# Optimization experiments

Measured on AMD Instinct MI355X. Metric: run time of the kernel, lower is better.

Reference implementation:

```python
import jax, jax.numpy as jnp
import numpy as np

CONV_DIMS = (-3, -2)   # spatial dims (channel-last layout)
RADIUS = (3, 3)        # window = 1 + 2*r = 7 per dim -> 49 cells
STEP = (1, 1)


def _unfold(x, dim, window, step):
    """torch.Tensor.unfold: dim -> out_len, window appended as last axis."""
    dim = dim % x.ndim
    n = x.shape[dim]
    starts = jnp.arange((n - window) // step + 1) * step          # [L]
    idx = starts[:, None] + jnp.arange(window)[None, :]           # [L, w]
    y = jnp.take(x, idx, axis=dim)                                # dim -> [L, w]
    return jnp.moveaxis(y, dim + 1, -1)                           # window axis to last


def _local_attention(x):
    # Unfold each conv dim; move its window axis to the front (as in the torch code).
    for i, r, s in zip(CONV_DIMS, RADIUS, STEP):
        x = _unfold(x, i, 1 + 2 * r, s)
        x = jnp.moveaxis(x, -1, 0)
    n_win = len(CONV_DIMS)
    cells = int(np.prod(x.shape[:n_win]))
    x = x.reshape((cells,) + x.shape[n_win:])      # [cells, B, H', W', C]
    center = cells // 2                            # spatial center of the window
    q = jnp.moveaxis(x[center:center + 1], 0, -2)  # [B, H', W', 1, C]
    k = jnp.moveaxis(jnp.concatenate([x[:center], x[center + 1:]], axis=0), 0, -2)  # [B,H',W',cells-1,C]
    d = q.shape[-1]
    scores = jnp.einsum('...qc,...kc->...qk', q, k) / jnp.sqrt(jnp.asarray(d, q.dtype))
    w = jax.nn.softmax(scores, axis=-1)
    out = jnp.einsum('...qk,...kc->...qc', w, k)   # keys double as values
    return out.squeeze(-2)                          # [B, H', W', C]


def setup_inputs() -> dict:
    key = jax.random.key(0)
    X = jax.random.normal(key, (4, 64, 64, 256), dtype=jnp.float32)
    return {"X": X}


def reference(X):
    return _local_attention(X)
```

## Files before the change

### kernel.cpp

```cpp
#include <hip/hip_runtime.h>
#include <hip/hip_bf16.h>

#define B_   4
#define H_   64
#define W_   64
#define C_   256
#define HO_  58
#define WO_  58
#define JT   4
#define GRID (B_ * HO_ * JT)
#define PERX (GRID / 8)
#define CH   136

typedef __attribute__((ext_vector_type(8))) short bf16x8;
typedef __attribute__((ext_vector_type(4))) float f32x4;

__device__ __forceinline__ unsigned pk2(float a, float b) {
    float2 t; t.x = a; t.y = b;
    __hip_bfloat162 h = __float22bfloat162_rn(t);
    union { __hip_bfloat162 h2; unsigned u; } cv; cv.h2 = h;
    return cv.u;
}

template <int CTRL>
__device__ __forceinline__ float dpp_add(float p) {
    int t = __builtin_amdgcn_update_dpp(0, __builtin_bit_cast(int, p),
                                        CTRL, 0xF, 0xF, true);
    return p + __builtin_bit_cast(float, t);
}

union FU { unsigned u[4]; bf16x8 f; };

__global__ __launch_bounds__(256, 2) void convnd_attn_kernel(const float* __restrict__ X,
                                                             float* __restrict__ out) {
    __shared__ unsigned short Kb[154 * CH];
    __shared__ float S[16 * 168];
    __shared__ float invS[16];
    __shared__ unsigned short Wt[7 * 16 * 32];

    const int sp = (blockIdx.x & 7) * PERX + (blockIdx.x >> 3);
    const int jt = sp & 3;
    const int t1 = sp >> 2;
    const int i  = t1 % HO_;
    const int b  = t1 / HO_;
    const int j0 = (jt == 3) ? 42 : jt * 16;

    const int tid  = threadIdx.x;
    const int wave = tid >> 6;
    const int lane = tid & 63;
    const int q4   = lane >> 4;
    const int m16  = lane & 15;
    const float* base = X + (size_t)b * H_ * W_ * C_;

    for (int z = tid; z < 7 * 16 * 32 / 2; z += 256) ((unsigned*)Wt)[z] = 0u;

    f32x4 accS[2][2];
    #pragma unroll
    for (int sl = 0; sl < 2; ++sl)
        #pragma unroll
        for (int nt = 0; nt < 2; ++nt)
            accS[sl][nt] = (f32x4){0.f, 0.f, 0.f, 0.f};

    #pragma unroll
    for (int p = 0; p < 2; ++p) {
        if (p) __syncthreads();
        for (int s = 0; s < 20; ++s) {
            const int e4 = s * 256 + tid;
            if (e4 < 154 * 32) {
                const int row = e4 >> 5;
                const int cw  = (e4 & 31) << 2;
                const int di  = (row * 187) >> 12;
                const int kx  = row - 22 * di;
                const float4 v = *(const float4*)&base[((size_t)((i + di) * W_ + (j0 + kx))) * C_ + (p << 7) + cw];
                uint2 u; u.x = pk2(v.x, v.y); u.y = pk2(v.z, v.w);
                *(uint2*)&Kb[row * CH + cw] = u;
            }
        }
        __syncthreads();

        bf16x8 aq[4];
        #pragma unroll
        for (int kk = 0; kk < 4; ++kk)
            aq[kk] = *(const bf16x8*)&Kb[(69 + m16) * CH + kk * 32 + q4 * 8];

        #pragma unroll
        for (int sl = 0; sl < 2; ++sl) {
            const int di = wave + sl * 4;
            if (di > 6) continue;
            #pragma unroll
            for (int nt = 0; nt < 2; ++nt) {
                const int n0 = nt * 6;
                #pragma unroll
                for (int kk = 0; kk < 4; ++kk) {
                    const bf16x8 bk = *(const bf16x8*)&Kb[(di * 22 + n0 + m16) * CH + kk * 32 + q4 * 8];
                    accS[sl][nt] = __builtin_amdgcn_mfma_f32_16x16x32_bf16(aq[kk], bk, accS[sl][nt], 0, 0, 0);
                }
            }
        }
    }

    #pragma unroll
    for (int sl = 0; sl < 2; ++sl) {
        const int di = wave + sl * 4;
        if (di > 6) continue;
        #pragma unroll
        for (int nt = 0; nt < 2; ++nt) {
            const int n0 = nt * 6;
            #pragma unroll
            for (int reg = 0; reg < 4; ++reg)
                S[(q4 * 4 + reg) * 168 + di * 24 + n0 + m16] = accS[sl][nt][reg] * 0.0625f;
        }
    }
    __syncthreads();

    const int px = wave * 4 + q4;
    float ev[4];
    float esum = 0.f;
    #pragma unroll
    for (int r = 0; r < 4; ++r) {
        const int cidx = m16 + r * 16;
        float e = 0.f;
        if (cidx < 49 && cidx != 24) {
            const int di = (cidx * 37) >> 8;
            const int dj = cidx - 7 * di;
            e = __expf(S[px * 168 + di * 24 + (px + dj)]);
        }
        ev[r] = e; esum += e;
    }
    esum = dpp_add<0x111>(esum);
    esum = dpp_add<0x112>(esum);
    esum = dpp_add<0x114>(esum);
    esum = dpp_add<0x118>(esum);
    if (m16 == 15) invS[px] = 1.f / esum;
    __syncthreads();
    {
        const float inv = invS[px];
        #pragma unroll
        for (int r = 0; r < 4; ++r) {
            const int cidx = m16 + r * 16;
            if (cidx < 49 && cidx != 24) {
                const int di = (cidx * 37) >> 8;
                const int dj = cidx - 7 * di;
                const unsigned wb = pk2(ev[r] * inv, 0.f);
                Wt[di * 512 + px * 32 + (px + dj)] = (unsigned short)(wb & 0xFFFFu);
            }
        }
    }
    __syncthreads();

    bf16x8 aw[7];
    #pragma unroll
    for (int di = 0; di < 7; ++di)
        aw[di] = *(const bf16x8*)&Wt[di * 512 + m16 * 32 + q4 * 8];

    const size_t ob = ((size_t)(b * HO_ + i) * WO_ + j0) * C_;
    #pragma unroll
    for (int nt = 0; nt < 4; ++nt) {
        const int c = wave * 64 + nt * 16 + m16;
        f32x4 acc = (f32x4){0.f, 0.f, 0.f, 0.f};
        #pragma unroll
        for (int di = 0; di < 7; ++di) {
            FU bu;
            if (q4 == 3) {
                bu.u[0] = 0u; bu.u[1] = 0u; bu.u[2] = 0u; bu.u[3] = 0u;
            } else {
                const float* rb = base + ((size_t)((i + di) * W_ + j0)) * C_ + c;
                float f[8];
                #pragma unroll
                for (int jj = 0; jj < 8; ++jj) {
                    const int kx  = q4 * 8 + jj;
                    const int kxc = (kx < 22) ? kx : 21;
                    f[jj] = rb[(size_t)kxc * C_];
                }
                bu.u[0] = pk2(f[0], f[1]); bu.u[1] = pk2(f[2], f[3]);
                bu.u[2] = pk2(f[4], f[5]); bu.u[3] = pk2(f[6], f[7]);
            }
            acc = __builtin_amdgcn_mfma_f32_16x16x32_bf16(aw[di], bu.f, acc, 0, 0, 0);
        }
        #pragma unroll
        for (int reg = 0; reg < 4; ++reg)
            out[ob + (size_t)(q4 * 4 + reg) * C_ + c] = acc[reg];
    }
}

extern "C" void kernel_launch(void* const* d_in, const int* in_sizes, int n_in,
                              void* d_out, int out_size, void* d_ws, size_t ws_size,
                              hipStream_t stream) {
    const float* X = (const float*)d_in[0];
    float* outp    = (float*)d_out;
    hipLaunchKernelGGL(convnd_attn_kernel, dim3(GRID), dim3(256), 0, stream, X, outp);
}
```

Measured before the change: 95.77 us.

## Rewrite tile as 8-column block with swizzled LDS keys reused for values

```diff
diff --git a/kernel.cpp b/kernel.cpp
--- a/kernel.cpp
+++ b/kernel.cpp
@@ -7,10 +7,8 @@
 #define C_   256
 #define HO_  58
 #define WO_  58
-#define JT   4
-#define GRID (B_ * HO_ * JT)
+#define GRID (B_ * HO_ * 8)
 #define PERX (GRID / 8)
-#define CH   136
 
 typedef __attribute__((ext_vector_type(8))) short bf16x8;
 typedef __attribute__((ext_vector_type(4))) float f32x4;
@@ -21,29 +19,27 @@
     union { __hip_bfloat162 h2; unsigned u; } cv; cv.h2 = h;
     return cv.u;
 }
-
-template <int CTRL>
-__device__ __forceinline__ float dpp_add(float p) {
-    int t = __builtin_amdgcn_update_dpp(0, __builtin_bit_cast(int, p),
-                                        CTRL, 0xF, 0xF, true);
-    return p + __builtin_bit_cast(float, t);
+__device__ __forceinline__ float bf16f(unsigned bits) {
+    return __builtin_bit_cast(float, bits << 16);
 }
-
+__device__ __forceinline__ int SWZ(int row, int e) {
+    return (row << 8) + ((((e) >> 3) ^ (row & 7)) << 3) + ((e) & 7);
+}
 union FU { unsigned u[4]; bf16x8 f; };
 
-__global__ __launch_bounds__(256, 2) void convnd_attn_kernel(const float* __restrict__ X,
+__global__ __launch_bounds__(256, 3) void convnd_attn_kernel(const float* __restrict__ X,
                                                              float* __restrict__ out) {
-    __shared__ unsigned short Kb[154 * CH];
-    __shared__ float S[16 * 168];
-    __shared__ float invS[16];
-    __shared__ unsigned short Wt[7 * 16 * 32];
+    __shared__ __align__(16) unsigned short Kb[98 * 256];
+    __shared__ __align__(16) unsigned short S16[98 * 8];
+    __shared__ __align__(16) unsigned short Wt[8 * 96];
+    __shared__ float Wtail[2 * 16];
 
     const int sp = (blockIdx.x & 7) * PERX + (blockIdx.x >> 3);
-    const int jt = sp & 3;
-    const int t1 = sp >> 2;
+    const int jt = sp & 7;
+    const int t1 = sp >> 3;
     const int i  = t1 % HO_;
     const int b  = t1 / HO_;
-    const int j0 = (jt == 3) ? 42 : jt * 16;
+    const int j0 = (jt == 7) ? 50 : jt * 8;
 
     const int tid  = threadIdx.x;
     const int wave = tid >> 6;
@@ -52,134 +48,135 @@
     const int m16  = lane & 15;
     const float* base = X + (size_t)b * H_ * W_ * C_;
 
-    for (int z = tid; z < 7 * 16 * 32 / 2; z += 256) ((unsigned*)Wt)[z] = 0u;
-
-    f32x4 accS[2][2];
-    #pragma unroll
-    for (int sl = 0; sl < 2; ++sl)
-        #pragma unroll
-        for (int nt = 0; nt < 2; ++nt)
-            accS[sl][nt] = (f32x4){0.f, 0.f, 0.f, 0.f};
-
-    #pragma unroll
-    for (int p = 0; p < 2; ++p) {
-        if (p) __syncthreads();
-        for (int s = 0; s < 20; ++s) {
-            const int e4 = s * 256 + tid;
-            if (e4 < 154 * 32) {
-                const int row = e4 >> 5;
-                const int cw  = (e4 & 31) << 2;
-                const int di  = (row * 187) >> 12;
-                const int kx  = row - 22 * di;
-                const float4 v = *(const float4*)&base[((size_t)((i + di) * W_ + (j0 + kx))) * C_ + (p << 7) + cw];
-                uint2 u; u.x = pk2(v.x, v.y); u.y = pk2(v.z, v.w);
-                *(uint2*)&Kb[row * CH + cw] = u;
-            }
-        }
-        __syncthreads();
-
-        bf16x8 aq[4];
-        #pragma unroll
-        for (int kk = 0; kk < 4; ++kk)
-            aq[kk] = *(const bf16x8*)&Kb[(69 + m16) * CH + kk * 32 + q4 * 8];
-
-        #pragma unroll
-        for (int sl = 0; sl < 2; ++sl) {
-            const int di = wave + sl * 4;
-            if (di > 6) continue;
-            #pragma unroll
-            for (int nt = 0; nt < 2; ++nt) {
-                const int n0 = nt * 6;
-                #pragma unroll
-                for (int kk = 0; kk < 4; ++kk) {
-                    const bf16x8 bk = *(const bf16x8*)&Kb[(di * 22 + n0 + m16) * CH + kk * 32 + q4 * 8];
-                    accS[sl][nt] = __builtin_amdgcn_mfma_f32_16x16x32_bf16(aq[kk], bk, accS[sl][nt], 0, 0, 0);
-                }
-            }
-        }
-    }
-
-    #pragma unroll
-    for (int sl = 0; sl < 2; ++sl) {
-        const int di = wave + sl * 4;
-        if (di > 6) continue;
-        #pragma unroll
-        for (int nt = 0; nt < 2; ++nt) {
-            const int n0 = nt * 6;
-            #pragma unroll
-            for (int reg = 0; reg < 4; ++reg)
-                S[(q4 * 4 + reg) * 168 + di * 24 + n0 + m16] = accS[sl][nt][reg] * 0.0625f;
+    #pragma unroll 5
+    for (int s = 0; s < 25; ++s) {
+        const int idx = s * 256 + tid;
+        if (idx < 6272) {
+            const int row = idx >> 6;
+            const int ch  = (idx & 63) << 2;
+            const int di  = (row * 2341) >> 15;
+            const int kx  = row - 14 * di;
+            const float4 v = *(const float4*)&base[((size_t)((i + di) * W_ + (j0 + kx))) * C_ + ch];
+            uint2 u; u.x = pk2(v.x, v.y); u.y = pk2(v.z, v.w);
+            *(uint2*)&Kb[SWZ(row, ch)] = u;
         }
     }
     __syncthreads();
 
-    const int px = wave * 4 + q4;
-    float ev[4];
-    float esum = 0.f;
+    const int rq = 45 + m16;
+    bf16x8 qf[8];
     #pragma unroll
-    for (int r = 0; r < 4; ++r) {
-        const int cidx = m16 + r * 16;
-        float e = 0.f;
-        if (cidx < 49 && cidx != 24) {
-            const int di = (cidx * 37) >> 8;
-            const int dj = cidx - 7 * di;
-            e = __expf(S[px * 168 + di * 24 + (px + dj)]);
+    for (int kk = 0; kk < 8; ++kk)
+        qf[kk] = *(const bf16x8*)&Kb[SWZ(rq, (kk << 5) + (q4 << 3))];
+
+    f32x4 accS[2];
+    accS[0] = (f32x4){0.f, 0.f, 0.f, 0.f};
+    accS[1] = (f32x4){0.f, 0.f, 0.f, 0.f};
+    #pragma unroll
+    for (int sl = 0; sl < 2; ++sl) {
+        const int di = wave + 4 * sl;
+        if (di > 6) continue;
+        const int rk = di * 14 + (m16 < 14 ? m16 : 13);
+        #pragma unroll
+        for (int kk = 0; kk < 8; ++kk) {
+            const bf16x8 kf_ = *(const bf16x8*)&Kb[SWZ(rk, (kk << 5) + (q4 << 3))];
+            accS[sl] = __builtin_amdgcn_mfma_f32_16x16x32_bf16(kf_, qf[kk], accS[sl], 0, 0, 0);
         }
-        ev[r] = e; esum += e;
     }
-    esum = dpp_add<0x111>(esum);
-    esum = dpp_add<0x112>(esum);
-    esum = dpp_add<0x114>(esum);
-    esum = dpp_add<0x118>(esum);
-    if (m16 == 15) invS[px] = 1.f / esum;
-    __syncthreads();
-    {
-        const float inv = invS[px];
+    #pragma unroll
+    for (int sl = 0; sl < 2; ++sl) {
+        const int di = wave + 4 * sl;
+        if (di > 6) continue;
         #pragma unroll
-        for (int r = 0; r < 4; ++r) {
-            const int cidx = m16 + r * 16;
-            if (cidx < 49 && cidx != 24) {
-                const int di = (cidx * 37) >> 8;
-                const int dj = cidx - 7 * di;
-                const unsigned wb = pk2(ev[r] * inv, 0.f);
-                Wt[di * 512 + px * 32 + (px + dj)] = (unsigned short)(wb & 0xFFFFu);
+        for (int reg = 0; reg < 4; ++reg) {
+            const int kx = (q4 << 2) + reg;
+            if (m16 < 8 && kx < 14) {
+                const float e = __expf(accS[sl][reg] * 0.0625f);
+                S16[(di * 14 + kx) * 8 + m16] = (unsigned short)(pk2(e, 0.f) & 0xFFFFu);
             }
         }
     }
     __syncthreads();
 
-    bf16x8 aw[7];
+    if (tid < 128) {
+        const int px  = tid >> 4;
+        const int l16 = tid & 15;
+        float vals[7], sum = 0.f;
+        #pragma unroll
+        for (int r = 0; r < 7; ++r) {
+            const int c = 16 * r + l16;
+            float e = 0.f;
+            if (c < 98) {
+                const int di = (c * 2341) >> 15;
+                const int dj = c - 14 * di - px;
+                if (dj >= 0 && dj <= 6 && !(di == 3 && dj == 3))
+                    e = bf16f(S16[c * 8 + px]);
+            }
+            vals[r] = e; sum += e;
+        }
+        sum += __shfl_xor(sum, 1, 64); sum += __shfl_xor(sum, 2, 64);
+        sum += __shfl_xor(sum, 4, 64); sum += __shfl_xor(sum, 8, 64);
+        const float inv = 1.f / sum;
+        #pragma unroll
+        for (int r = 0; r < 7; ++r) {
+            const int c = 16 * r + l16;
+            if (c < 96)       Wt[px * 96 + c] = (unsigned short)(pk2(vals[r] * inv, 0.f) & 0xFFFFu);
+            else if (c < 98)  Wtail[(c - 96) * 16 + px] = vals[r] * inv;
+        }
+    }
+    __syncthreads();
+
+    bf16x8 aW[3];
     #pragma unroll
-    for (int di = 0; di < 7; ++di)
-        aw[di] = *(const bf16x8*)&Wt[di * 512 + m16 * 32 + q4 * 8];
+    for (int kf = 0; kf < 3; ++kf)
+        aW[kf] = *(const bf16x8*)&Wt[(m16 & 7) * 96 + (kf << 5) + (q4 << 3)];
+
+    const int ep = (wave << 6) + (m16 << 1);
+    f32x4 aE[2], aO[2];
+    aE[0] = aE[1] = aO[0] = aO[1] = (f32x4){0.f, 0.f, 0.f, 0.f};
+    #pragma unroll
+    for (int p = 0; p < 2; ++p) {
+        const int e = ep + (p << 5);
+        #pragma unroll
+        for (int kf = 0; kf < 3; ++kf) {
+            unsigned u[8];
+            #pragma unroll
+            for (int jj = 0; jj < 8; ++jj) {
+                const int cell = (kf << 5) + (q4 << 3) + jj;
+                u[jj] = *(const unsigned*)&Kb[SWZ(cell, e)];
+            }
+            FU fE, fO;
+            #pragma unroll
+            for (int j2 = 0; j2 < 4; ++j2) {
+                fE.u[j2] = __builtin_amdgcn_perm(u[2 * j2 + 1], u[2 * j2], 0x05040100u);
+                fO.u[j2] = __builtin_amdgcn_perm(u[2 * j2 + 1], u[2 * j2], 0x07060302u);
+            }
+            aE[p] = __builtin_amdgcn_mfma_f32_16x16x32_bf16(aW[kf], fE.f, aE[p], 0, 0, 0);
+            aO[p] = __builtin_amdgcn_mfma_f32_16x16x32_bf16(aW[kf], fO.f, aO[p], 0, 0, 0);
+        }
+        const unsigned u96 = *(const unsigned*)&Kb[SWZ(96, e)];
+        const unsigned u97 = *(const unsigned*)&Kb[SWZ(97, e)];
+        const float E96 = bf16f(u96 & 0xFFFFu), O96 = bf16f(u96 >> 16);
+        const float E97 = bf16f(u97 & 0xFFFFu), O97 = bf16f(u97 >> 16);
+        #pragma unroll
+        for (int reg = 0; reg < 4; ++reg) {
+            const int px = (q4 << 2) + reg;
+            const float w6 = Wtail[px], w7 = Wtail[16 + px];
+            aE[p][reg] = fmaf(w6, E96, fmaf(w7, E97, aE[p][reg]));
+            aO[p][reg] = fmaf(w6, O96, fmaf(w7, O97, aO[p][reg]));
+        }
+    }
 
     const size_t ob = ((size_t)(b * HO_ + i) * WO_ + j0) * C_;
-    #pragma unroll
-    for (int nt = 0; nt < 4; ++nt) {
-        const int c = wave * 64 + nt * 16 + m16;
-        f32x4 acc = (f32x4){0.f, 0.f, 0.f, 0.f};
+    if (q4 < 2) {
         #pragma unroll
-        for (int di = 0; di < 7; ++di) {
-            FU bu;
-            if (q4 == 3) {
-                bu.u[0] = 0u; bu.u[1] = 0u; bu.u[2] = 0u; bu.u[3] = 0u;
-            } else {
-                const float* rb = base + ((size_t)((i + di) * W_ + j0)) * C_ + c;
-                float f[8];
-                #pragma unroll
-                for (int jj = 0; jj < 8; ++jj) {
-                    const int kx  = q4 * 8 + jj;
-                    const int kxc = (kx < 22) ? kx : 21;
-                    f[jj] = rb[(size_t)kxc * C_];
-                }
-                bu.u[0] = pk2(f[0], f[1]); bu.u[1] = pk2(f[2], f[3]);
-                bu.u[2] = pk2(f[4], f[5]); bu.u[3] = pk2(f[6], f[7]);
+        for (int p = 0; p < 2; ++p)
+            #pragma unroll
+            for (int reg = 0; reg < 4; ++reg) {
+                const int px = (q4 << 2) + reg;
+                float2 o; o.x = aE[p][reg]; o.y = aO[p][reg];
+                *(float2*)&out[ob + (size_t)px * C_ + (wave << 6) + (p << 5) + (m16 << 1)] = o;
             }
-            acc = __builtin_amdgcn_mfma_f32_16x16x32_bf16(aw[di], bu.f, acc, 0, 0, 0);
-        }
-        #pragma unroll
-        for (int reg = 0; reg < 4; ++reg)
-            out[ob + (size_t)(q4 * 4 + reg) * C_ + c] = acc[reg];
     }
 }
 
```

Result: faster. 91.95 us (-4.0%).
